# Kernel optimization log

Measured on AMD Instinct MI355X. Metric: run time of the kernel, lower is better.

Reference implementation:

```python
import jax, jax.numpy as jnp
import numpy as np

B_, N, C, H, WS, NW = 2048, 49, 384, 12, 7, 64
D = C // H  # head_dim = 32
SCALE = D ** -0.5


def _relative_position_index(ws=WS):
    coords = np.stack(np.meshgrid(np.arange(ws), np.arange(ws), indexing='ij'))  # [2,ws,ws]
    flat = coords.reshape(2, -1)                         # [2, N]
    rel = flat[:, :, None] - flat[:, None, :]            # [2, N, N]
    rel = rel.transpose(1, 2, 0)                         # [N, N, 2]
    rel[..., 0] += ws - 1
    rel[..., 1] += ws - 1
    rel[..., 0] *= 2 * ws - 1
    return rel.sum(-1).astype(np.int32)                  # [N, N]


def setup_inputs() -> dict:
    key = jax.random.key(0)
    ks = jax.random.split(key, 9)
    return {
        'x1': jax.random.normal(ks[0], (B_, N, C), jnp.float32),
        'x2': jax.random.normal(ks[1], (B_, N, C), jnp.float32),
        'mask1': jax.random.normal(ks[2], (NW, N, N), jnp.float32),
        'mask2': jax.random.normal(ks[3], (NW, N, N), jnp.float32),
        'w_qkv': jax.random.normal(ks[4], (C, 3 * C), jnp.float32) * 0.02,
        'b_qkv': jax.random.normal(ks[5], (3 * C,), jnp.float32) * 0.02,
        'w_proj': jax.random.normal(ks[6], (C, C), jnp.float32) * 0.02,
        'b_proj': jax.random.normal(ks[7], (C,), jnp.float32) * 0.02,
        'rpb_table': jax.random.normal(ks[8], ((2 * WS - 1) ** 2, H), jnp.float32) * 0.02,
        'rel_index': jnp.asarray(_relative_position_index()),
    }


def _qkv(x, w_qkv, b_qkv):
    # x: [B_, N, C] -> q,k,v each [B_, H, N, D]
    qkv = (x @ w_qkv + b_qkv).reshape(B_, N, 3, H, D).transpose(2, 0, 3, 1, 4)
    return qkv[0], qkv[1], qkv[2]


def reference(x1, x2, mask1, mask2, w_qkv, b_qkv, w_proj, b_proj, rpb_table, rel_index):
    # relative position bias: [H, N, N]
    rpb = rpb_table[rel_index.reshape(-1)].reshape(N, N, H).transpose(2, 0, 1)

    q1, k1, v1 = _qkv(x1, w_qkv, b_qkv)
    _, k2, v2 = _qkv(x2, w_qkv, b_qkv)
    q1s = q1 * SCALE

    attn1 = jnp.einsum('bhnd,bhmd->bhnm', q1s, k1) + rpb[None]
    attn2 = jnp.einsum('bhnd,bhmd->bhnm', q1s, k2) + rpb[None]  # note: q1, per source

    # shifted-window mask add: [B_//nW, nW, H, N, N] + mask[None, :, None]
    attn1 = (attn1.reshape(B_ // NW, NW, H, N, N) + mask1[None, :, None]).reshape(B_, H, N, N)
    attn2 = (attn2.reshape(B_ // NW, NW, H, N, N) + mask2[None, :, None]).reshape(B_, H, N, N)

    attn = jax.nn.softmax(jnp.concatenate([attn1, attn2], axis=1), axis=-1)  # [B_, 2H, N, N]

    v = jnp.concatenate([v1, v2], axis=1)  # [B_, 2H, N, D]
    out = jnp.einsum('bhnm,bhmd->bhnd', attn, v)
    weights = out.transpose(0, 2, 1, 3).reshape(B_, N, 2 * C)
    x = weights[:, :, :C] @ w_proj + b_proj
    return x, weights
```

## Files before the change

### kernel.cpp

```cpp
#include <hip/hip_runtime.h>

typedef unsigned short u16;
typedef unsigned int u32;
typedef __attribute__((ext_vector_type(8))) short short8;
typedef __attribute__((ext_vector_type(4))) float f32x4;

#define NB 2048
#define NTOK 49
#define CH 384
#define NH 12
#define HD 32
#define SCALE_Q 0.17677669529663687f
#define TABF 1956864

__device__ __forceinline__ u16 f2bf(float f) {
  u32 u = __float_as_uint(f);
  u += 0x7fffu + ((u >> 16) & 1u);
  return (u16)(u >> 16);
}
__device__ __forceinline__ float bf2f(u16 h) { return __uint_as_float(((u32)h) << 16); }
__device__ __forceinline__ u32 pk2(float a, float b) { return (u32)f2bf(a) | ((u32)f2bf(b) << 16); }

__device__ __forceinline__ void gload16(const u16* g, u16* l) {
  __builtin_amdgcn_global_load_lds(
      (const __attribute__((address_space(1))) u32*)g,
      (__attribute__((address_space(3))) u32*)l,
      16, 0, 0);
}

__global__ __launch_bounds__(256) void prep_all(
    const float* __restrict__ x1, const float* __restrict__ x2,
    u16* __restrict__ xb1, u16* __restrict__ xb2,
    const float* __restrict__ w_qkv, const float* __restrict__ w_proj,
    u16* __restrict__ wqkvT, u16* __restrict__ wprojT,
    const float* __restrict__ rpb_table, const int* __restrict__ rel_index,
    const float* __restrict__ mask1, const float* __restrict__ mask2,
    float* __restrict__ comb)
{
  const int bid = blockIdx.x;
  if (bid < 18816) {
    const size_t i = ((size_t)bid * 256 + threadIdx.x) * 8;
    float4 a = *reinterpret_cast<const float4*>(x1 + i);
    float4 b = *reinterpret_cast<const float4*>(x1 + i + 4);
    uint4 o;
    o.x = pk2(a.x, a.y); o.y = pk2(a.z, a.w); o.z = pk2(b.x, b.y); o.w = pk2(b.z, b.w);
    *reinterpret_cast<uint4*>(xb1 + i) = o;
    a = *reinterpret_cast<const float4*>(x2 + i);
    b = *reinterpret_cast<const float4*>(x2 + i + 4);
    o.x = pk2(a.x, a.y); o.y = pk2(a.z, a.w); o.z = pk2(b.x, b.y); o.w = pk2(b.z, b.w);
    *reinterpret_cast<uint4*>(xb2 + i) = o;
  } else if (bid < 18816 + 2304) {
    int idx = (bid - 18816) * 256 + threadIdx.x;
    if (idx < 1152 * 384) {
      int n = idx / 384, k = idx - n * 384;
      wqkvT[idx] = f2bf(w_qkv[(size_t)k * 1152 + n]);
    } else if (idx < 1152 * 384 + 384 * 384) {
      int i2 = idx - 1152 * 384;
      int n = i2 / 384, k = i2 - n * 384;
      wprojT[i2] = f2bf(w_proj[(size_t)k * 384 + n]);
    }
  } else {
    const int wbh = bid - (18816 + 2304);
    const int wb = wbh / 12, h = wbh - wb * 12;
    const size_t ob = (size_t)wbh * (49 * 52);
    for (int r = threadIdx.x; r < 2401; r += 256) {
      int i = r / 49, j = r - i * 49;
      float rv = rpb_table[(size_t)rel_index[r] * 12 + h];
      comb[ob + i * 52 + j]        = rv + mask1[(size_t)wb * 2401 + r];
      comb[TABF + ob + i * 52 + j] = rv + mask2[(size_t)wb * 2401 + r];
    }
  }
}

__global__ __launch_bounds__(512) void gemm_qkv(
    const u16* __restrict__ xb1, const u16* __restrict__ xb2,
    const u16* __restrict__ wT, const float* __restrict__ bias,
    u16* __restrict__ q1, u16* __restrict__ k1, u16* __restrict__ v1,
    u16* __restrict__ k2, u16* __restrict__ v2)
{
  __shared__ __align__(16) u16 smem[38912];
  u16* Cs = smem;

  const int bid0 = blockIdx.x;
  const int lin = (bid0 & 7) * 735 + (bid0 >> 3);
  const int mt = lin / 15;
  const int nt = lin - mt * 15;

  const bool isx2 = nt >= 9;
  const u16* __restrict__ X = isx2 ? xb2 : xb1;
  const int colbase = isx2 ? 384 + (nt - 9) * 128 : nt * 128;
  const int m0 = mt * 256;
  const int tid = threadIdx.x;
  const int lane = tid & 63, w = tid >> 6;
  const int wm = w & 3, wn = w >> 2;
  const int l15 = lane & 15, l4 = lane >> 4;

  f32x4 acc[4][4] = {};

  const u16* ga = X + (size_t)(m0 + l15) * CH + l4 * 8;
  const u16* gb = wT + (size_t)(colbase + w * 16 + l15) * CH + l4 * 8;
  const int ga0 = (2 * w) * 16 * CH, ga1 = (2 * w + 1) * 16 * CH;

  auto stage = [&](int bs, int kk) {
    u16* A = smem + bs * 12288;
    u16* B = A + 8192;
    gload16(ga + kk + ga0, &A[(2 * w) * 512]);
    gload16(ga + kk + ga1, &A[(2 * w + 1) * 512]);
    gload16(gb + kk, &B[w * 512]);
  };

  stage(0, 0);
  stage(1, 32);
  stage(2, 64);

#pragma unroll
  for (int k = 0; k < 12; ++k) {
    if (k == 0)       asm volatile("s_waitcnt vmcnt(6)" ::: "memory");
    else if (k <= 10) asm volatile("s_waitcnt vmcnt(3)" ::: "memory");
    else              asm volatile("s_waitcnt vmcnt(0)" ::: "memory");
    __builtin_amdgcn_s_barrier();
    __builtin_amdgcn_sched_barrier(0);
    if (k >= 1 && k + 2 < 12)
      stage((k - 1) % 3, (k + 2) * 32);
    const int cb = k % 3;
    const u16* A = smem + cb * 12288;
    const u16* B = A + 8192;
    short8 af[4], bfr[4];
#pragma unroll
    for (int i = 0; i < 4; ++i)
      af[i] = *reinterpret_cast<const short8*>(&A[(wm * 4 + i) * 512 + lane * 8]);
#pragma unroll
    for (int j = 0; j < 4; ++j)
      bfr[j] = *reinterpret_cast<const short8*>(&B[(wn * 4 + j) * 512 + lane * 8]);
#pragma unroll
    for (int i = 0; i < 4; ++i)
#pragma unroll
      for (int j = 0; j < 4; ++j)
        acc[i][j] = __builtin_amdgcn_mfma_f32_16x16x32_bf16(af[i], bfr[j], acc[i][j], 0, 0, 0);
  }

  asm volatile("s_waitcnt lgkmcnt(0)" ::: "memory");
  __builtin_amdgcn_s_barrier();
#pragma unroll
  for (int j = 0; j < 4; ++j) {
    const int colL = wn * 64 + j * 16 + l15;
    const int gcol = colbase + colL;
    const float bb = bias[gcol];
    const float scl = (gcol < 384) ? SCALE_Q : 1.0f;
#pragma unroll
    for (int i = 0; i < 4; ++i)
#pragma unroll
      for (int r = 0; r < 4; ++r) {
        const int row = wm * 64 + i * 16 + l4 * 4 + r;
        Cs[row * 152 + (colL ^ (((row >> 2) & 3) << 3))] = f2bf((acc[i][j][r] + bb) * scl);
      }
  }
  __syncthreads();

  u16* dst;
  int tb;
  if (colbase < 384)      { dst = q1;              tb = colbase; }
  else if (colbase < 768) { dst = isx2 ? k2 : k1;  tb = colbase - 384; }
  else                    { dst = isx2 ? v2 : v1;  tb = colbase - 768; }

#pragma unroll
  for (int u = 0; u < 8; ++u) {
    const int pc = tid + u * 512;
    const int row = pc >> 4, pp = pc & 15;
    const uint4 val = *reinterpret_cast<const uint4*>(&Cs[row * 152 + ((pp ^ ((row >> 2) & 3)) << 3)]);
    const int gm = m0 + row;
    const int b = gm / 49, tok = gm - b * 49;
    const int cm = tb + pp * 8;
    const int h = cm >> 5, d0 = cm & 31;
    *reinterpret_cast<uint4*>(&dst[(((size_t)b * NH + h) * NTOK + tok) * HD + d0]) = val;
  }
}

__global__ __launch_bounds__(256) void attn_kernel(
    const u16* __restrict__ q1, const u16* __restrict__ k1, const u16* __restrict__ v1,
    const u16* __restrict__ k2, const u16* __restrict__ v2,
    const float* __restrict__ comb, float* __restrict__ outw)
{
  __shared__ __align__(16) u16 VT[2][32][72];
  __shared__ __align__(16) u16 Pb[4][2][2][512];

  const int h = blockIdx.x, b = blockIdx.y;
  const int tid = threadIdx.x;
  const int lane = tid & 63, wt = tid >> 6;
  const int l15 = lane & 15, l4 = lane >> 4;
  const size_t base = ((size_t)b * NH + h) * 1568;

  for (int e = tid; e < 392; e += 256) {
    const int p = e >= 196;
    const int e2 = e - p * 196;
    const int tok = e2 >> 2, d8 = (e2 & 3) * 8;
    const u16* src = (p ? v2 : v1) + base + tok * 32 + d8;
    uint4 val = *reinterpret_cast<const uint4*>(src);
    const u16* pv = reinterpret_cast<const u16*>(&val);
#pragma unroll
    for (int q = 0; q < 8; ++q) VT[p][d8 + q][tok] = pv[q];
  }
  for (int e = tid; e < 2 * 32 * 15; e += 256) {
    int p = (e >= 480) ? 1 : 0;
    int e2 = e - p * 480;
    int d = e2 / 15, j = 49 + (e2 - d * 15);
    VT[p][d][j] = 0;
  }

  const short8 aq = *reinterpret_cast<const short8*>(&q1[base + (wt * 16 + l15) * 32 + l4 * 8]);

  __syncthreads();

  const int wb = b & 63;
  const int irow = wt * 16 + l15;
  const float* cb0 = comb + ((size_t)(wb * 12 + h) * 49 + (irow < 49 ? irow : 48)) * 52;
  const size_t obase = (size_t)b * (NTOK * 768) + (size_t)h * 32;

#pragma unroll
  for (int p = 0; p < 2; ++p) {
    const u16* __restrict__ kp = p ? k2 : k1;
    const float* cbp = cb0 + (size_t)p * TABF;

    f32x4 st[4];
    __builtin_amdgcn_s_setprio(1);
#pragma unroll
    for (int jt = 0; jt < 4; ++jt) {
      short8 bk = *reinterpret_cast<const short8*>(&kp[base + (jt * 16 + l15) * 32 + l4 * 8]);
      st[jt] = __builtin_amdgcn_mfma_f32_16x16x32_bf16(bk, aq, (f32x4){0.f, 0.f, 0.f, 0.f}, 0, 0, 0);
    }
    __builtin_amdgcn_s_setprio(0);

#pragma unroll
    for (int jt = 0; jt < 4; ++jt) {
      const float4 c = *reinterpret_cast<const float4*>(cbp + jt * 16 + l4 * 4);
#pragma unroll
      for (int r = 0; r < 4; ++r) {
        const int j = jt * 16 + l4 * 4 + r;
        st[jt][r] = (j < 49) ? st[jt][r] + (&c.x)[r] : -1e30f;
      }
    }

    float mx = -1e30f;
#pragma unroll
    for (int jt = 0; jt < 4; ++jt)
#pragma unroll
      for (int r = 0; r < 4; ++r) mx = fmaxf(mx, st[jt][r]);
    mx = fmaxf(mx, __shfl_xor(mx, 16));
    mx = fmaxf(mx, __shfl_xor(mx, 32));
    float sm = 0.f;
#pragma unroll
    for (int jt = 0; jt < 4; ++jt)
#pragma unroll
      for (int r = 0; r < 4; ++r) {
        float e = __expf(st[jt][r] - mx);
        st[jt][r] = e;
        sm += e;
      }
    sm += __shfl_xor(sm, 16);
    sm += __shfl_xor(sm, 32);
    const float si = 1.f / sm;

#pragma unroll
    for (int jt = 0; jt < 4; ++jt) {
      const int kt = jt >> 1;
#pragma unroll
      for (int r = 0; r < 4; r += 2) {
        const u32 pkv = pk2(st[jt][r] * si, st[jt][r + 1] * si);
        const int jrel = (jt & 1) * 16 + l4 * 4 + r;
        const int off = ((jrel >> 3) << 7) + l15 * 8 + (jrel & 7);
        *reinterpret_cast<u32*>(&Pb[wt][p][kt][off]) = pkv;
      }
    }

    f32x4 o[2] = {};
    __builtin_amdgcn_s_setprio(1);
#pragma unroll
    for (int kt = 0; kt < 2; ++kt) {
      short8 ap = *reinterpret_cast<const short8*>(&Pb[wt][p][kt][lane * 8]);
#pragma unroll
      for (int n2 = 0; n2 < 2; ++n2) {
        short8 bvf = *reinterpret_cast<const short8*>(&VT[p][n2 * 16 + l15][kt * 32 + l4 * 8]);
        o[n2] = __builtin_amdgcn_mfma_f32_16x16x32_bf16(bvf, ap, o[n2], 0, 0, 0);
      }
    }
    __builtin_amdgcn_s_setprio(0);

    const int i = wt * 16 + l15;
    if (i < 49) {
#pragma unroll
      for (int n2 = 0; n2 < 2; ++n2) {
        float4 vst = {o[n2][0], o[n2][1], o[n2][2], o[n2][3]};
        *reinterpret_cast<float4*>(&outw[obase + (size_t)i * 768 + p * 384 + n2 * 16 + l4 * 4]) = vst;
      }
    }
  }
}

__global__ __launch_bounds__(256) void gemm_proj(
    const float* __restrict__ Wsrc, const u16* __restrict__ wT,
    const float* __restrict__ bias, float* __restrict__ outx)
{
  __shared__ __align__(16) u16 smem[24576];
  const int bid0 = blockIdx.x;
  const int lin = (bid0 & 7) * 294 + (bid0 >> 3);
  const int mt = lin / 3;
  const int nt = lin - mt * 3;

  const int colbase = nt * 128;
  const int m0 = mt * 128;
  const int tid = threadIdx.x;
  const int lane = tid & 63, wv = tid >> 6;
  const int wr = wv >> 1, wc = wv & 1;
  const int l15 = lane & 15, l4 = lane >> 4;

  f32x4 acc[4][4] = {};

  const float* ga = Wsrc + (size_t)(m0 + l15) * 768 + l4 * 8;
  const u16*   gb = wT + (size_t)(colbase + l15) * CH + l4 * 8;
  const int g0 = wv, g1 = wv + 4;

  float4 ar0[2][2], ar1[2][2], ar2[2][2];
  auto loadA = [&](float4 (*ar)[2], int kk) {
    ar[0][0] = *reinterpret_cast<const float4*>(ga + kk + g0 * 16 * 768);
    ar[0][1] = *reinterpret_cast<const float4*>(ga + kk + g0 * 16 * 768 + 4);
    ar[1][0] = *reinterpret_cast<const float4*>(ga + kk + g1 * 16 * 768);
    ar[1][1] = *reinterpret_cast<const float4*>(ga + kk + g1 * 16 * 768 + 4);
  };
  auto stageB = [&](int bs, int kk) {
    u16* B = smem + bs * 8192 + 4096;
    gload16(gb + kk + g0 * 16 * CH, B + g0 * 512);
    gload16(gb + kk + g1 * 16 * CH, B + g1 * 512);
  };
  auto writeA = [&](float4 (*ar)[2], int bs) {
    u16* A = smem + bs * 8192;
    uint4 v;
    v.x = pk2(ar[0][0].x, ar[0][0].y); v.y = pk2(ar[0][0].z, ar[0][0].w);
    v.z = pk2(ar[0][1].x, ar[0][1].y); v.w = pk2(ar[0][1].z, ar[0][1].w);
    *reinterpret_cast<uint4*>(&A[g0 * 512 + lane * 8]) = v;
    v.x = pk2(ar[1][0].x, ar[1][0].y); v.y = pk2(ar[1][0].z, ar[1][0].w);
    v.z = pk2(ar[1][1].x, ar[1][1].y); v.w = pk2(ar[1][1].z, ar[1][1].w);
    *reinterpret_cast<uint4*>(&A[g1 * 512 + lane * 8]) = v;
  };

  loadA(ar0, 0);  stageB(0, 0);
  loadA(ar1, 32); stageB(1, 32);
  loadA(ar2, 64); stageB(2, 64);

#pragma unroll
  for (int k = 0; k < 12; ++k) {
    if (k <= 9)       asm volatile("s_waitcnt vmcnt(12)" ::: "memory");
    else if (k == 10) asm volatile("s_waitcnt vmcnt(6)" ::: "memory");
    else              asm volatile("s_waitcnt vmcnt(0)" ::: "memory");
    const int cb = k % 3;
    if (cb == 0) writeA(ar0, 0);
    else if (cb == 1) writeA(ar1, 1);
    else writeA(ar2, 2);
    asm volatile("s_waitcnt lgkmcnt(0)" ::: "memory");
    __builtin_amdgcn_s_barrier();
    __builtin_amdgcn_sched_barrier(0);
    const u16* A = smem + cb * 8192;
    const u16* B = A + 4096;
    short8 af[4], bfr[4];
#pragma unroll
    for (int i = 0; i < 4; ++i)
      af[i] = *reinterpret_cast<const short8*>(&A[(wr * 4 + i) * 512 + lane * 8]);
#pragma unroll
    for (int j = 0; j < 4; ++j)
      bfr[j] = *reinterpret_cast<const short8*>(&B[(wc * 4 + j) * 512 + lane * 8]);
#pragma unroll
    for (int i = 0; i < 4; ++i)
#pragma unroll
      for (int j = 0; j < 4; ++j)
        acc[i][j] = __builtin_amdgcn_mfma_f32_16x16x32_bf16(af[i], bfr[j], acc[i][j], 0, 0, 0);
    asm volatile("s_waitcnt lgkmcnt(0)" ::: "memory");
    __builtin_amdgcn_s_barrier();
    __builtin_amdgcn_sched_barrier(0);
    if (k + 3 < 12) {
      if (cb == 0)      loadA(ar0, (k + 3) * 32);
      else if (cb == 1) loadA(ar1, (k + 3) * 32);
      else              loadA(ar2, (k + 3) * 32);
      stageB(cb, (k + 3) * 32);
    }
  }

#pragma unroll
  for (int j = 0; j < 4; ++j) {
    const int col = colbase + wc * 64 + j * 16 + l15;
    const float bb = bias[col];
#pragma unroll
    for (int i = 0; i < 4; ++i) {
#pragma unroll
      for (int r = 0; r < 4; ++r) {
        const int gm = m0 + wr * 64 + i * 16 + l4 * 4 + r;
        outx[(size_t)gm * CH + col] = acc[i][j][r] + bb;
      }
    }
  }
}

extern "C" void kernel_launch(void* const* d_in, const int* in_sizes, int n_in,
                              void* d_out, int out_size, void* d_ws, size_t ws_size,
                              hipStream_t stream) {
  const float* x1        = (const float*)d_in[0];
  const float* x2        = (const float*)d_in[1];
  const float* mask1     = (const float*)d_in[2];
  const float* mask2     = (const float*)d_in[3];
  const float* w_qkv     = (const float*)d_in[4];
  const float* b_qkv     = (const float*)d_in[5];
  const float* w_proj    = (const float*)d_in[6];
  const float* b_proj    = (const float*)d_in[7];
  const float* rpb_table = (const float*)d_in[8];
  const int*   rel_index = (const int*)d_in[9];

  float* outx = (float*)d_out;
  const size_t SZe = (size_t)NB * NH * NTOK * HD;
  float* outw = outx + SZe;

  u16* q1 = (u16*)d_out;
  u16* k1 = q1 + SZe;
  u16* xb1 = (u16*)outw;
  u16* xb2 = xb1 + SZe;

  u16* v1 = (u16*)d_ws;
  u16* k2 = v1 + SZe;
  u16* v2 = k2 + SZe;
  u16* wqkvT  = v2 + SZe;
  u16* wprojT = wqkvT + 1152 * 384;
  float* comb = (float*)(wprojT + 384 * 384);

  prep_all<<<21888, 256, 0, stream>>>(x1, x2, xb1, xb2, w_qkv, w_proj, wqkvT, wprojT,
                                      rpb_table, rel_index, mask1, mask2, comb);
  gemm_qkv<<<5880, 512, 0, stream>>>(xb1, xb2, wqkvT, b_qkv, q1, k1, v1, k2, v2);
  attn_kernel<<<dim3(12, 2048), 256, 0, stream>>>(q1, k1, v1, k2, v2, comb, outw);
  gemm_proj<<<2352, 256, 0, stream>>>(outw, wprojT, b_proj, outx);
}
```

Before: 722.2 us.

## Load QKV GEMM operands directly into registers, dropping LDS staging

The QKV projection GEMM no longer stages A/B tiles through LDS with a triple-buffered global_load_lds pipeline. Each wave now loads its own MFMA fragments straight from global memory into registers, double-buffered across k-steps, and the per-iteration barriers go away. This removes LDS traffic and synchronisation, but waves in the same row or column of the block now each fetch their shared A and B tiles from memory separately, which increases global/L2 load traffic and register pressure.

```diff
diff --git a/kernel.cpp b/kernel.cpp
--- a/kernel.cpp
+++ b/kernel.cpp
@@ -78,8 +78,7 @@
     u16* __restrict__ q1, u16* __restrict__ k1, u16* __restrict__ v1,
     u16* __restrict__ k2, u16* __restrict__ v2)
 {
-  __shared__ __align__(16) u16 smem[38912];
-  u16* Cs = smem;
+  __shared__ __align__(16) u16 Cs[38912];
 
   const int bid0 = blockIdx.x;
   const int lin = (bid0 & 7) * 735 + (bid0 >> 3);
@@ -95,52 +94,45 @@
   const int wm = w & 3, wn = w >> 2;
   const int l15 = lane & 15, l4 = lane >> 4;
 
+  const u16* ga = X + (size_t)(m0 + wm * 64 + l15) * CH + l4 * 8;
+  const u16* gb = wT + (size_t)(colbase + wn * 64 + l15) * CH + l4 * 8;
+
+  short8 a0[4], a1[4], b0[4], b1[4];
+  auto loadA = [&](short8* ar, int kk) {
+#pragma unroll
+    for (int i = 0; i < 4; ++i)
+      ar[i] = *reinterpret_cast<const short8*>(ga + i * 16 * CH + kk);
+  };
+  auto loadB = [&](short8* br, int kk) {
+#pragma unroll
+    for (int j = 0; j < 4; ++j)
+      br[j] = *reinterpret_cast<const short8*>(gb + j * 16 * CH + kk);
+  };
+
+  loadA(a0, 0);  loadB(b0, 0);
+  loadA(a1, 32); loadB(b1, 32);
+
   f32x4 acc[4][4] = {};
-
-  const u16* ga = X + (size_t)(m0 + l15) * CH + l4 * 8;
-  const u16* gb = wT + (size_t)(colbase + w * 16 + l15) * CH + l4 * 8;
-  const int ga0 = (2 * w) * 16 * CH, ga1 = (2 * w + 1) * 16 * CH;
-
-  auto stage = [&](int bs, int kk) {
-    u16* A = smem + bs * 12288;
-    u16* B = A + 8192;
-    gload16(ga + kk + ga0, &A[(2 * w) * 512]);
-    gload16(ga + kk + ga1, &A[(2 * w + 1) * 512]);
-    gload16(gb + kk, &B[w * 512]);
-  };
-
-  stage(0, 0);
-  stage(1, 32);
-  stage(2, 64);
-
 #pragma unroll
   for (int k = 0; k < 12; ++k) {
-    if (k == 0)       asm volatile("s_waitcnt vmcnt(6)" ::: "memory");
-    else if (k <= 10) asm volatile("s_waitcnt vmcnt(3)" ::: "memory");
-    else              asm volatile("s_waitcnt vmcnt(0)" ::: "memory");
-    __builtin_amdgcn_s_barrier();
-    __builtin_amdgcn_sched_barrier(0);
-    if (k >= 1 && k + 2 < 12)
-      stage((k - 1) % 3, (k + 2) * 32);
-    const int cb = k % 3;
-    const u16* A = smem + cb * 12288;
-    const u16* B = A + 8192;
-    short8 af[4], bfr[4];
-#pragma unroll
-    for (int i = 0; i < 4; ++i)
-      af[i] = *reinterpret_cast<const short8*>(&A[(wm * 4 + i) * 512 + lane * 8]);
-#pragma unroll
-    for (int j = 0; j < 4; ++j)
-      bfr[j] = *reinterpret_cast<const short8*>(&B[(wn * 4 + j) * 512 + lane * 8]);
-#pragma unroll
-    for (int i = 0; i < 4; ++i)
-#pragma unroll
-      for (int j = 0; j < 4; ++j)
-        acc[i][j] = __builtin_amdgcn_mfma_f32_16x16x32_bf16(af[i], bfr[j], acc[i][j], 0, 0, 0);
-  }
-
-  asm volatile("s_waitcnt lgkmcnt(0)" ::: "memory");
-  __builtin_amdgcn_s_barrier();
+    if ((k & 1) == 0) {
+#pragma unroll
+      for (int i = 0; i < 4; ++i)
+#pragma unroll
+        for (int j = 0; j < 4; ++j)
+          acc[i][j] = __builtin_amdgcn_mfma_f32_16x16x32_bf16(a0[i], b0[j], acc[i][j], 0, 0, 0);
+      if (k + 2 < 12) { loadA(a0, (k + 2) * 32); loadB(b0, (k + 2) * 32); }
+    } else {
+#pragma unroll
+      for (int i = 0; i < 4; ++i)
+#pragma unroll
+        for (int j = 0; j < 4; ++j)
+          acc[i][j] = __builtin_amdgcn_mfma_f32_16x16x32_bf16(a1[i], b1[j], acc[i][j], 0, 0, 0);
+      if (k + 2 < 12) { loadA(a1, (k + 2) * 32); loadB(b1, (k + 2) * 32); }
+    }
+  }
+
+  __syncthreads();
 #pragma unroll
   for (int j = 0; j < 4; ++j) {
     const int colL = wn * 64 + j * 16 + l15;
```

Result: slower. 994.4 us (+37.7%).
